# Performance work log

Measured on AMD Instinct MI355X. Metric: run time of the kernel, lower is better.

Reference implementation:

```python
import jax, jax.numpy as jnp
import numpy as np

DIM = 1024
NUM_HEADS = 16
HEAD_DIM = DIM // NUM_HEADS
BATCH = 2
SEQ = 2048
ROPE_BASE = 10000.0


def _rope_cos_sin(seq_len, head_dim, dtype=jnp.float32):
    inv_freq = 1.0 / (ROPE_BASE ** (jnp.arange(0, head_dim, 2, dtype=jnp.float32) / head_dim))
    t = jnp.arange(seq_len, dtype=jnp.float32)
    freqs = jnp.outer(t, inv_freq)              # (S, D/2)
    emb = jnp.concatenate([freqs, freqs], axis=-1)  # (S, D)
    return jnp.cos(emb).astype(dtype), jnp.sin(emb).astype(dtype)


def _rotate_half(x):
    x1, x2 = jnp.split(x, 2, axis=-1)
    return jnp.concatenate([-x2, x1], axis=-1)


def _apply_rope(x, cos, sin):
    # x: (B, S, H, D); cos/sin: (S, D) -> broadcast (1, S, 1, D)
    cos = cos[None, :, None, :]
    sin = sin[None, :, None, :]
    return x * cos + _rotate_half(x) * sin


def setup_inputs() -> dict:
    key = jax.random.key(0)
    ks = jax.random.split(key, 5)
    x = jax.random.normal(ks[0], (BATCH, SEQ, DIM), dtype=jnp.float32)
    scale = DIM ** -0.5
    wq = jax.random.normal(ks[1], (DIM, DIM), dtype=jnp.float32) * scale
    wk = jax.random.normal(ks[2], (DIM, DIM), dtype=jnp.float32) * scale
    wv = jax.random.normal(ks[3], (DIM, DIM), dtype=jnp.float32) * scale
    wo = jax.random.normal(ks[4], (DIM, DIM), dtype=jnp.float32) * scale
    return {"x": x, "wq": wq, "wk": wk, "wv": wv, "wo": wo}


def reference(x, wq, wk, wv, wo):
    B, S, _ = x.shape
    scale = HEAD_DIM ** -0.5
    # nn.Linear(x) = x @ W.T; weights stored (out, in)
    q = (x @ wq.T).reshape(B, S, NUM_HEADS, HEAD_DIM)
    k = (x @ wk.T).reshape(B, S, NUM_HEADS, HEAD_DIM)
    v = (x @ wv.T).reshape(B, S, NUM_HEADS, HEAD_DIM)
    cos, sin = _rope_cos_sin(S, HEAD_DIM, x.dtype)
    q = _apply_rope(q, cos, sin)
    k = _apply_rope(k, cos, sin)
    # (B, H, S, S) scores, full softmax attention (no mask, dropout=0)
    scores = jnp.einsum('bqhd,bkhd->bhqk', q, k) * scale
    attn = jax.nn.softmax(scores, axis=-1)
    out = jnp.einsum('bhqk,bkhd->bqhd', attn, v).reshape(B, S, DIM)
    return out @ wo.T
```

## Files before the change

### kernel.cpp

```cpp
#include <hip/hip_runtime.h>
#include <hip/hip_bf16.h>
#include <stdint.h>


#define AS1(p) ((const __attribute__((address_space(1))) void*)(p))
#define AS3(p) ((__attribute__((address_space(3))) void*)(p))

typedef __attribute__((ext_vector_type(8)))  __bf16 bf16x8;
typedef __attribute__((ext_vector_type(4)))  float  f32x4;
typedef __attribute__((ext_vector_type(16))) float  f32x16;

__device__ __forceinline__ ushort f2b(float f) {
  union { float f; uint32_t u; } v; v.f = f;
  uint32_t u = v.u;
  u += 0x7fffu + ((u >> 16) & 1);
  return (ushort)(u >> 16);
}
__device__ __forceinline__ float b2f(ushort s) {
  union { uint32_t u; float f; } v; v.u = ((uint32_t)s) << 16;
  return v.f;
}
__device__ __forceinline__ uint32_t pkbf16(float lo, float hi) {
  uint32_t w;
  asm("v_cvt_pk_bf16_f32 %0, %1, %2" : "=v"(w) : "v"(lo), "v"(hi));
  return w;
}
__device__ __forceinline__ float fast_exp2(float x) {
#if __has_builtin(__builtin_amdgcn_exp2f)
  return __builtin_amdgcn_exp2f(x);
#else
  float r;
  asm("v_exp_f32 %0, %1\n\ts_nop 1" : "=v"(r) : "v"(x));
  return r;
#endif
}

__global__ __launch_bounds__(256) void cvt_all_k(
    const float* __restrict__ x,  const float* __restrict__ wq,
    const float* __restrict__ wk, const float* __restrict__ wv,
    const float* __restrict__ wo, ushort* __restrict__ dst) {
  int i = blockIdx.x * 256 + threadIdx.x;
  const float* src;
  if      (i < 1048576) src = x  + (size_t)i * 4;
  else if (i < 1310720) src = wq + (size_t)(i - 1048576) * 4;
  else if (i < 1572864) src = wk + (size_t)(i - 1310720) * 4;
  else if (i < 1835008) src = wv + (size_t)(i - 1572864) * 4;
  else                  src = wo + (size_t)(i - 1835008) * 4;
  float4 v = *(const float4*)src;
  ushort4 o;
  o.x = f2b(v.x); o.y = f2b(v.y); o.z = f2b(v.z); o.w = f2b(v.w);
  ((ushort4*)dst)[i] = o;
}

__device__ __forceinline__ void gemm_mainloop(
    const ushort* __restrict__ A, const ushort* __restrict__ W,
    int row0, int col0, ushort* lds, f32x4 acc[4][4]) {
  const int K = 1024;
  int tid = threadIdx.x;
  int lane = tid & 63, wid = tid >> 6;
  int wr = wid >> 1, wc = wid & 1;
  int lr = lane >> 4, lc = lane & 15;
  ushort* lA = lds;
  ushort* lB = lds + 8192;

  auto stage = [&](int buf, int k0) {
#pragma unroll
    for (int i = 0; i < 2; i++) {
      int idx = tid + i * 256;
      const ushort* ga = A + (size_t)(row0 + (idx >> 2)) * K + k0 + (idx & 3) * 8;
      __builtin_amdgcn_global_load_lds(AS1(ga),
          AS3(lA + buf * 4096 + (i * 256 + wid * 64) * 8), 16, 0, 0);
      const ushort* gb = W + (size_t)(col0 + (idx >> 2)) * K + k0 + (idx & 3) * 8;
      __builtin_amdgcn_global_load_lds(AS1(gb),
          AS3(lB + buf * 4096 + (i * 256 + wid * 64) * 8), 16, 0, 0);
    }
  };

  stage(0, 0);
  __syncthreads();
  int cur = 0;
  for (int k0 = 0; k0 < K; k0 += 32) {
    if (k0 + 32 < K) stage(cur ^ 1, k0 + 32);
    const ushort* a  = lA + cur * 4096;
    const ushort* bm = lB + cur * 4096;
    bf16x8 af[4], bfr[4];
#pragma unroll
    for (int m = 0; m < 4; m++)
      af[m] = *(const bf16x8*)(a + (wr * 64 + m * 16 + lc) * 32 + lr * 8);
#pragma unroll
    for (int n = 0; n < 4; n++)
      bfr[n] = *(const bf16x8*)(bm + (wc * 64 + n * 16 + lc) * 32 + lr * 8);
#pragma unroll
    for (int m = 0; m < 4; m++)
#pragma unroll
      for (int n = 0; n < 4; n++)
        acc[m][n] = __builtin_amdgcn_mfma_f32_16x16x32_bf16(af[m], bfr[n], acc[m][n], 0, 0, 0);
    __syncthreads();
    cur ^= 1;
  }
}

__global__ __launch_bounds__(256) void gemm_qkv_k(
    const ushort* __restrict__ xb,
    const ushort* __restrict__ wqb, const ushort* __restrict__ wkb,
    const ushort* __restrict__ wvb,
    ushort* __restrict__ Qb, ushort* __restrict__ Kb, ushort* __restrict__ Vtb) {
  __shared__ ushort lds[16384];
  int z = blockIdx.z;
  const ushort* w = (z == 0) ? wqb : (z == 1) ? wkb : wvb;
  int row0 = blockIdx.x * 128, col0 = blockIdx.y * 128;
  f32x4 acc[4][4] = {};
  gemm_mainloop(xb, w, row0, col0, lds, acc);

  int tid = threadIdx.x, lane = tid & 63, wid = tid >> 6;
  int wr = wid >> 1, wc = wid & 1, lr = lane >> 4, lc = lane & 15;

  if (z < 2) {
    ushort* dst = (z == 0) ? Qb : Kb;
#pragma unroll
    for (int m = 0; m < 4; m++)
#pragma unroll
      for (int n = 0; n < 4; n++)
#pragma unroll
        for (int j = 0; j < 4; j++) {
          int i = row0 + wr * 64 + m * 16 + lr * 4 + j;
          int c = col0 + wc * 64 + n * 16 + lc;
          int b = i >> 11, s = i & 2047, h = c >> 6, d = c & 63;
          dst[(size_t)(b * 16 + h) * 131072 + (size_t)s * 64 + d] = f2b(acc[m][n][j]);
        }
  } else {
#pragma unroll
    for (int m = 0; m < 4; m++)
#pragma unroll
      for (int n = 0; n < 4; n++) {
        int c = wc * 64 + n * 16 + lc;
        int sb = wr * 64 + m * 16 + lr * 4;
        uint32_t w0 = pkbf16(acc[m][n][0], acc[m][n][1]);
        uint32_t w1 = pkbf16(acc[m][n][2], acc[m][n][3]);
        int soff = sb ^ ((c & 7) << 3);
        uint2 val; val.x = w0; val.y = w1;
        *(uint2*)(lds + c * 128 + soff) = val;
      }
    __syncthreads();
    int b = row0 >> 11, srow = row0 & 2047;
#pragma unroll
    for (int i = 0; i < 8; i++) {
      int idx = i * 256 + tid;
      int cl = idx >> 4, sc = idx & 15;
      int soff = (sc * 8) ^ ((cl & 7) << 3);
      bf16x8 v = *(const bf16x8*)(lds + cl * 128 + soff);
      int cg = col0 + cl, h = cg >> 6, d = cg & 63;
      *(bf16x8*)(Vtb + (size_t)(b * 16 + h) * 131072 + (size_t)d * 2048 + srow + sc * 8) = v;
    }
  }
}

__global__ __launch_bounds__(256) void gemm_out_k(
    const ushort* __restrict__ Ab, const ushort* __restrict__ wob,
    float* __restrict__ out) {
  __shared__ ushort lds[16384];
  int row0 = blockIdx.x * 128, col0 = blockIdx.y * 128;
  f32x4 acc[4][4] = {};
  gemm_mainloop(Ab, wob, row0, col0, lds, acc);

  int tid = threadIdx.x, lane = tid & 63, wid = tid >> 6;
  int wr = wid >> 1, wc = wid & 1, lr = lane >> 4, lc = lane & 15;
#pragma unroll
  for (int m = 0; m < 4; m++)
#pragma unroll
    for (int n = 0; n < 4; n++)
#pragma unroll
      for (int j = 0; j < 4; j++) {
        int i = row0 + wr * 64 + m * 16 + lr * 4 + j;
        int c = col0 + wc * 64 + n * 16 + lc;
        out[(size_t)i * 1024 + c] = acc[m][n][j];
      }
}

__global__ __launch_bounds__(256) void rope_k(ushort* __restrict__ Qb,
                                              ushort* __restrict__ Kb) {
  const float QSCL = 0.125f * 1.44269504088896f;
  int idx = blockIdx.x * 256 + threadIdx.x;
  int dp = idx & 31;
  int s  = (idx >> 5) & 2047;
  int bh = idx >> 16;
  float inv = exp2f((float)dp * (-13.2877123795494f / 32.0f));
  float ang = (float)s * inv;
  float sn, cs;
  sincosf(ang, &sn, &cs);
  size_t off = (size_t)bh * 131072 + (size_t)s * 64 + dp;
  float q1 = b2f(Qb[off]), q2 = b2f(Qb[off + 32]);
  Qb[off]      = f2b((q1 * cs - q2 * sn) * QSCL);
  Qb[off + 32] = f2b((q2 * cs + q1 * sn) * QSCL);
  float k1 = b2f(Kb[off]), k2 = b2f(Kb[off + 32]);
  Kb[off]      = f2b(k1 * cs - k2 * sn);
  Kb[off + 32] = f2b(k2 * cs + k1 * sn);
}

__global__ __launch_bounds__(256, 3) void attn_k(
    const ushort* __restrict__ Qb, const ushort* __restrict__ Kb,
    const ushort* __restrict__ Vtb, ushort* __restrict__ Ob) {
  __shared__ ushort kvlds[2][2][4096];
  int tid = threadIdx.x, lane = tid & 63, wid = tid >> 6;
  int lc5 = lane & 31, hi = lane >> 5;

  int bid = blockIdx.x;
  int qt = (bid >> 3) & 15;
  int bh = (bid & 7) + ((bid >> 7) << 3);
  int q0 = qt * 128 + wid * 32;
  const ushort* Qp = Qb  + (size_t)bh * 131072 + (size_t)q0 * 64;
  const ushort* Kp = Kb  + (size_t)bh * 131072;
  const ushort* Vp = Vtb + (size_t)bh * 131072;

  bf16x8 qf[4];
#pragma unroll
  for (int ks = 0; ks < 4; ks++)
    qf[ks] = *(const bf16x8*)(Qp + lc5 * 64 + ks * 16 + hi * 8);

  f32x16 o0, o1;
#pragma unroll
  for (int i = 0; i < 16; i++) { o0[i] = 0.f; o1[i] = 0.f; }
  float lsum = 0.f;

  int swz[4];
#pragma unroll
  for (int ks = 0; ks < 4; ks++)
    swz[ks] = (((2 * ks + hi) ^ (lc5 & 7)) << 4);
  const int rbase = lc5 * 128;

  auto stage = [&](int buf, int kv) {
#pragma unroll
    for (int i = 0; i < 2; i++) {
      int idx = i * 256 + tid;
      int r = idx >> 3, cp = idx & 7;
      int ubase = (i * 256 + wid * 64) * 16;
      const ushort* gk = Kp + (size_t)(kv + r) * 64 + ((cp ^ (r & 7)) << 3);
      __builtin_amdgcn_global_load_lds(AS1(gk),
          AS3((char*)&kvlds[buf][0][0] + ubase), 16, 0, 0);
      const ushort* gv = Vp + (size_t)r * 2048 + kv + ((cp ^ (r & 7)) << 3);
      __builtin_amdgcn_global_load_lds(AS1(gv),
          AS3((char*)&kvlds[buf][1][0] + ubase), 16, 0, 0);
    }
  };

  stage(0, 0);
  __syncthreads();
  int cur = 0;

  for (int kv = 0; kv < 2048; kv += 64) {
    if (kv + 64 < 2048) stage(cur ^ 1, kv + 64);
    const char* kbuf = (const char*)&kvlds[cur][0][0];
    const char* vbuf = (const char*)&kvlds[cur][1][0];

    f32x16 s0 = {}, s1 = {};
    __builtin_amdgcn_s_setprio(1);
#pragma unroll
    for (int ks = 0; ks < 4; ks++) {
      bf16x8 ka0 = *(const bf16x8*)(kbuf + rbase + swz[ks]);
      bf16x8 ka1 = *(const bf16x8*)(kbuf + 4096 + rbase + swz[ks]);
      s0 = __builtin_amdgcn_mfma_f32_32x32x16_bf16(ka0, qf[ks], s0, 0, 0, 0);
      s1 = __builtin_amdgcn_mfma_f32_32x32x16_bf16(ka1, qf[ks], s1, 0, 0, 0);
    }
    __builtin_amdgcn_s_setprio(0);

#pragma unroll
    for (int i = 0; i < 16; i++) {
      s0[i] = fast_exp2(s0[i]);
      s1[i] = fast_exp2(s1[i]);
    }
    float acc = 0.f;
#pragma unroll
    for (int i = 0; i < 16; i++) acc += s0[i] + s1[i];
    lsum += acc;

    bf16x8 a[4];
#pragma unroll
    for (int t = 0; t < 2; t++) {
      const f32x16& s = t ? s1 : s0;
#pragma unroll
      for (int h2 = 0; h2 < 2; h2++) {
        int rb = 8 * h2;
        uint32_t wa1 = pkbf16(s[rb],     s[rb + 1]);
        uint32_t wb1 = pkbf16(s[rb + 4], s[rb + 5]);
        asm("v_permlane32_swap_b32 %0, %1" : "+v"(wa1), "+v"(wb1));
        uint32_t wa2 = pkbf16(s[rb + 2], s[rb + 3]);
        uint32_t wb2 = pkbf16(s[rb + 6], s[rb + 7]);
        asm("v_permlane32_swap_b32 %0, %1" : "+v"(wa2), "+v"(wb2));
        union { uint32_t u[4]; bf16x8 v; } tmp;
        tmp.u[0] = wa1; tmp.u[1] = wa2; tmp.u[2] = wb1; tmp.u[3] = wb2;
        a[t * 2 + h2] = tmp.v;
      }
    }

    __builtin_amdgcn_s_setprio(1);
#pragma unroll
    for (int ks = 0; ks < 4; ks++) {
      bf16x8 vb0 = *(const bf16x8*)(vbuf + rbase + swz[ks]);
      bf16x8 vb1 = *(const bf16x8*)(vbuf + 4096 + rbase + swz[ks]);
      o0 = __builtin_amdgcn_mfma_f32_32x32x16_bf16(a[ks], vb0, o0, 0, 0, 0);
      o1 = __builtin_amdgcn_mfma_f32_32x32x16_bf16(a[ks], vb1, o1, 0, 0, 0);
    }
    __builtin_amdgcn_s_setprio(0);
    __syncthreads();
    cur ^= 1;
  }

  lsum += __shfl_xor(lsum, 32);
  float invq = 1.0f / lsum;
  float invr[16];
#pragma unroll
  for (int r = 0; r < 16; r++)
    invr[r] = __shfl(invq, (r & 3) + 8 * (r >> 2) + 4 * hi);

  int b = bh >> 4, h = bh & 15;
  ushort* Op = Ob + (size_t)(b * 2048 + q0) * 1024 + h * 64 + lc5;
#pragma unroll
  for (int r = 0; r < 16; r++) {
    int rrow = (r & 3) + 8 * (r >> 2) + 4 * hi;
    Op[(size_t)rrow * 1024]      = f2b(o0[r] * invr[r]);
    Op[(size_t)rrow * 1024 + 32] = f2b(o1[r] * invr[r]);
  }
}

extern "C" void kernel_launch(void* const* d_in, const int* in_sizes, int n_in,
                              void* d_out, int out_size, void* d_ws, size_t ws_size,
                              hipStream_t stream) {
  const float* x  = (const float*)d_in[0];
  const float* wq = (const float*)d_in[1];
  const float* wk = (const float*)d_in[2];
  const float* wv = (const float*)d_in[3];
  const float* wo = (const float*)d_in[4];
  float* out = (float*)d_out;
  char* ws = (char*)d_ws;
  const size_t MiB = 1024 * 1024;
  ushort* xb  = (ushort*)(ws + 0);
  ushort* wqb = (ushort*)(ws + 8 * MiB);
  ushort* wkb = (ushort*)(ws + 10 * MiB);
  ushort* wvb = (ushort*)(ws + 12 * MiB);
  ushort* wob = (ushort*)(ws + 14 * MiB);
  ushort* Qb  = (ushort*)(ws + 16 * MiB);
  ushort* Kb  = (ushort*)(ws + 24 * MiB);
  ushort* Vtb = (ushort*)(ws + 32 * MiB);
  ushort* Ob  = (ushort*)(ws + 40 * MiB);

  cvt_all_k<<<8192, 256, 0, stream>>>(x, wq, wk, wv, wo, xb);
  dim3 gqkv(32, 8, 3);
  gemm_qkv_k<<<gqkv, 256, 0, stream>>>(xb, wqb, wkb, wvb, Qb, Kb, Vtb);
  rope_k<<<8192, 256, 0, stream>>>(Qb, Kb);
  attn_k<<<512, 256, 0, stream>>>(Qb, Kb, Vtb, Ob);
  dim3 gout(32, 8);
  gemm_out_k<<<gout, 256, 0, stream>>>(Ob, wob, out);
}
```

Baseline: 113.1 us.

## Split attention KV range across two wave groups per block with LDS reduction

Doubles the attention block to 512 threads, with two groups of four waves that each cover the same 128 queries but take alternate 64-key halves of each 128-key tile. The LDS staging is widened to load 128 keys per iteration, and at the end the second group writes its partial O and row sums to LDS so the first group can add them before normalizing and storing. The aim is more waves in flight per block and half as many loop iterations per wave, hiding latency better. The cost is 64KB of LDS per block, which limits residency, plus a final reduction and barrier.

```diff
diff --git a/kernel.cpp b/kernel.cpp
--- a/kernel.cpp
+++ b/kernel.cpp
@@ -197,17 +197,18 @@
   Kb[off + 32] = f2b(k2 * cs + k1 * sn);
 }
 
-__global__ __launch_bounds__(256, 3) void attn_k(
+__global__ __launch_bounds__(512, 4) void attn_k(
     const ushort* __restrict__ Qb, const ushort* __restrict__ Kb,
     const ushort* __restrict__ Vtb, ushort* __restrict__ Ob) {
-  __shared__ ushort kvlds[2][2][4096];
+  __shared__ char ldsb[65536];
   int tid = threadIdx.x, lane = tid & 63, wid = tid >> 6;
   int lc5 = lane & 31, hi = lane >> 5;
+  int qsub = wid & 3, grp = wid >> 2;
 
   int bid = blockIdx.x;
   int qt = (bid >> 3) & 15;
   int bh = (bid & 7) + ((bid >> 7) << 3);
-  int q0 = qt * 128 + wid * 32;
+  int q0 = qt * 128 + qsub * 32;
   const ushort* Qp = Qb  + (size_t)bh * 131072 + (size_t)q0 * 64;
   const ushort* Kp = Kb  + (size_t)bh * 131072;
   const ushort* Vp = Vtb + (size_t)bh * 131072;
@@ -228,18 +229,16 @@
     swz[ks] = (((2 * ks + hi) ^ (lc5 & 7)) << 4);
   const int rbase = lc5 * 128;
 
-  auto stage = [&](int buf, int kv) {
-#pragma unroll
-    for (int i = 0; i < 2; i++) {
-      int idx = i * 256 + tid;
-      int r = idx >> 3, cp = idx & 7;
-      int ubase = (i * 256 + wid * 64) * 16;
-      const ushort* gk = Kp + (size_t)(kv + r) * 64 + ((cp ^ (r & 7)) << 3);
-      __builtin_amdgcn_global_load_lds(AS1(gk),
-          AS3((char*)&kvlds[buf][0][0] + ubase), 16, 0, 0);
-      const ushort* gv = Vp + (size_t)r * 2048 + kv + ((cp ^ (r & 7)) << 3);
-      __builtin_amdgcn_global_load_lds(AS1(gv),
-          AS3((char*)&kvlds[buf][1][0] + ubase), 16, 0, 0);
+  auto stage = [&](int buf, int kvp) {
+    int r = tid >> 3, cp = tid & 7;
+    int ubase = wid * 1024;
+#pragma unroll
+    for (int t = 0; t < 2; t++) {
+      char* tb = ldsb + buf * 32768 + t * 16384;
+      const ushort* gk = Kp + (size_t)(kvp + 64 * t + r) * 64 + ((cp ^ (r & 7)) << 3);
+      __builtin_amdgcn_global_load_lds(AS1(gk), AS3(tb + ubase), 16, 0, 0);
+      const ushort* gv = Vp + (size_t)r * 2048 + kvp + 64 * t + ((cp ^ (r & 7)) << 3);
+      __builtin_amdgcn_global_load_lds(AS1(gv), AS3(tb + 8192 + ubase), 16, 0, 0);
     }
   };
 
@@ -247,10 +246,10 @@
   __syncthreads();
   int cur = 0;
 
-  for (int kv = 0; kv < 2048; kv += 64) {
-    if (kv + 64 < 2048) stage(cur ^ 1, kv + 64);
-    const char* kbuf = (const char*)&kvlds[cur][0][0];
-    const char* vbuf = (const char*)&kvlds[cur][1][0];
+  for (int kvp = 0; kvp < 2048; kvp += 128) {
+    if (kvp + 128 < 2048) stage(cur ^ 1, kvp + 128);
+    const char* kbuf = ldsb + cur * 32768 + grp * 16384;
+    const char* vbuf = kbuf + 8192;
 
     f32x16 s0 = {}, s1 = {};
     __builtin_amdgcn_s_setprio(1);
@@ -305,20 +304,34 @@
     cur ^= 1;
   }
 
-  lsum += __shfl_xor(lsum, 32);
-  float invq = 1.0f / lsum;
-  float invr[16];
-#pragma unroll
-  for (int r = 0; r < 16; r++)
-    invr[r] = __shfl(invq, (r & 3) + 8 * (r >> 2) + 4 * hi);
-
-  int b = bh >> 4, h = bh & 15;
-  ushort* Op = Ob + (size_t)(b * 2048 + q0) * 1024 + h * 64 + lc5;
-#pragma unroll
-  for (int r = 0; r < 16; r++) {
-    int rrow = (r & 3) + 8 * (r >> 2) + 4 * hi;
-    Op[(size_t)rrow * 1024]      = f2b(o0[r] * invr[r]);
-    Op[(size_t)rrow * 1024 + 32] = f2b(o1[r] * invr[r]);
+  float* cb = (float*)ldsb;
+  float* p = cb + (size_t)(qsub * 64 + lane) * 33;
+  if (grp == 1) {
+#pragma unroll
+    for (int i = 0; i < 16; i++) { p[i] = o0[i]; p[16 + i] = o1[i]; }
+    p[32] = lsum;
+  }
+  __syncthreads();
+  if (grp == 0) {
+#pragma unroll
+    for (int i = 0; i < 16; i++) { o0[i] += p[i]; o1[i] += p[16 + i]; }
+    lsum += p[32];
+
+    lsum += __shfl_xor(lsum, 32);
+    float invq = 1.0f / lsum;
+    float invr[16];
+#pragma unroll
+    for (int r = 0; r < 16; r++)
+      invr[r] = __shfl(invq, (r & 3) + 8 * (r >> 2) + 4 * hi);
+
+    int b = bh >> 4, h = bh & 15;
+    ushort* Op = Ob + (size_t)(b * 2048 + q0) * 1024 + h * 64 + lc5;
+#pragma unroll
+    for (int r = 0; r < 16; r++) {
+      int rrow = (r & 3) + 8 * (r >> 2) + 4 * hi;
+      Op[(size_t)rrow * 1024]      = f2b(o0[r] * invr[r]);
+      Op[(size_t)rrow * 1024 + 32] = f2b(o1[r] * invr[r]);
+    }
   }
 }
 
@@ -347,7 +360,7 @@
   dim3 gqkv(32, 8, 3);
   gemm_qkv_k<<<gqkv, 256, 0, stream>>>(xb, wqb, wkb, wvb, Qb, Kb, Vtb);
   rope_k<<<8192, 256, 0, stream>>>(Qb, Kb);
-  attn_k<<<512, 256, 0, stream>>>(Qb, Kb, Vtb, Ob);
+  attn_k<<<512, 512, 0, stream>>>(Qb, Kb, Vtb, Ob);
   dim3 gout(32, 8);
   gemm_out_k<<<gout, 256, 0, stream>>>(Ob, wob, out);
 }
```

After: 110.9 us. 1.02x faster.
